# Performance work log

Hardware: AMD Instinct MI355X
Metric: run time of the kernel (lower is better)

The kernel has to match this reference:

```python
import jax, jax.numpy as jnp
import numpy as np

H = 768          # hidden_size
NH = 12          # num heads
HD = H // NH     # head dim
NEG = -1e9       # stand-in for -inf masked_fill (numerically safe)


def setup_inputs() -> dict:
    key = jax.random.key(0)
    ks = jax.random.split(key, 8)
    B, T = 4, 2048
    s = 0.02
    return {
        "hidden_states": jax.random.normal(ks[0], (B, T, H), jnp.float32),
        "attention_mask": jnp.zeros((B, 1, 1, T), jnp.float32),
        "Wq": jax.random.normal(ks[1], (H, H), jnp.float32) * s,
        "bq": jnp.zeros((H,), jnp.float32),
        "Wk": jax.random.normal(ks[2], (H, H), jnp.float32) * s,
        "bk": jnp.zeros((H,), jnp.float32),
        "Wv": jax.random.normal(ks[3], (H, H), jnp.float32) * s,
        "bv": jnp.zeros((H,), jnp.float32),
    }


def _split_heads(x):
    b, t, _ = x.shape
    return x.reshape(b, t, NH, HD).transpose(0, 2, 1, 3)  # b h t d


def reference(hidden_states, attention_mask, Wq, bq, Wk, bk, Wv, bv):
    q = _split_heads(hidden_states @ Wq.T + bq)
    k = _split_heads(hidden_states @ Wk.T + bk)
    v = _split_heads(hidden_states @ Wv.T + bv)
    T = q.shape[2]
    scores = jnp.einsum('bhid,bhjd->bhij', q, k) / jnp.sqrt(jnp.float32(HD))
    causal = jnp.tril(jnp.ones((T, T), bool))
    scores = jnp.where(causal, scores, NEG) + attention_mask
    probs = jax.nn.softmax(scores, axis=-1)
    out = jnp.einsum('bhij,bhjd->bhid', probs, v)
    b = out.shape[0]
    return out.transpose(0, 2, 1, 3).reshape(b, T, H)  # b t (h d)
```

## Files before the change

kernel.cpp:

```cpp
#include <hip/hip_runtime.h>
#include <hip/hip_bf16.h>

#define Tsz 2048
#define Hsz 768
#define NHsz 12
#define HDsz 64

typedef unsigned short u16;
typedef unsigned int u32;
typedef __attribute__((ext_vector_type(8))) short bf16x8;
typedef __attribute__((ext_vector_type(4))) float f32x4;
typedef __attribute__((ext_vector_type(4))) u16 u16x4;

__device__ __forceinline__ u16 f2bf(float f) {
    union { __hip_bfloat16 h; u16 u; } c;
    c.h = __float2bfloat16(f);
    return c.u;
}

__device__ __forceinline__ void glds16(const void* src, void* ldsbase) {
    __builtin_amdgcn_global_load_lds(
        (const __attribute__((address_space(1))) u32*)src,
        (__attribute__((address_space(3))) u32*)ldsbase, 16, 0, 0);
}

#define BAR() do { asm volatile("" ::: "memory"); \
                   __builtin_amdgcn_s_barrier();  \
                   asm volatile("" ::: "memory"); } while (0)

#define LDSFRAG(base, row, c) \
    (*(const bf16x8*)((const char*)(base) + (row)*128 + ((((c) << 4)) ^ (((row) & 7) << 4))))

__global__ __launch_bounds__(256) void to_bf16(
    const float* __restrict__ X,
    const float* __restrict__ Wq, const float* __restrict__ Wk,
    const float* __restrict__ Wv,
    u16* __restrict__ xb, u16* __restrict__ wb)
{
    const int bx = blockIdx.x, tid = threadIdx.x;
    const float* src;
    u16* dst;
    size_t off;
    if (bx < 768) {
        src = X; dst = xb;
        off = ((size_t)bx * 256 + tid) * 32;
    } else {
        int r = bx - 768;
        int wsel = r / 72, lr = r % 72;
        src = (wsel == 0) ? Wq : (wsel == 1) ? Wk : Wv;
        dst = wb + (size_t)wsel * (Hsz * Hsz);
        off = ((size_t)lr * 256 + tid) * 32;
    }
    #pragma unroll
    for (int c = 0; c < 4; ++c) {
        float4 a = *(const float4*)(src + off + c * 8);
        float4 b = *(const float4*)(src + off + c * 8 + 4);
        bf16x8 v;
        v[0] = (short)f2bf(a.x); v[1] = (short)f2bf(a.y);
        v[2] = (short)f2bf(a.z); v[3] = (short)f2bf(a.w);
        v[4] = (short)f2bf(b.x); v[5] = (short)f2bf(b.y);
        v[6] = (short)f2bf(b.z); v[7] = (short)f2bf(b.w);
        *(bf16x8*)(dst + off + c * 8) = v;
    }
}

__global__ __launch_bounds__(256) void qkv_gemm(
    const u16* __restrict__ xb, const u16* __restrict__ wb,
    const float* __restrict__ bq, const float* __restrict__ bk,
    const float* __restrict__ bv,
    u16* __restrict__ q_ws, u16* __restrict__ k_ws, u16* __restrict__ vt_ws)
{
    const int tid = threadIdx.x;
    const int w = tid >> 6, l = tid & 63, lg = l >> 4, lh = l & 15;
    const int nb = blockIdx.x;
    const int m0 = blockIdx.y * 128;
    const int z = nb / 6;
    const int n0l = (nb % 6) * 128;
    const u16* Wb = wb + (size_t)z * (Hsz * Hsz);
    const float* bias = (z == 0) ? bq : (z == 1) ? bk : bv;

    __shared__ __align__(16) u16 Xs[2][128 * 64];
    __shared__ __align__(16) u16 Ws[2][128 * 64];

    const int wm = w >> 1, wn = w & 1;

    f32x4 acc[4][4];
    #pragma unroll
    for (int i = 0; i < 4; ++i)
        #pragma unroll
        for (int j = 0; j < 4; ++j)
            acc[i][j] = (f32x4){0.f, 0.f, 0.f, 0.f};

    auto stage = [&](int buf, int k0) {
        #pragma unroll
        for (int p = 0; p < 4; ++p) {
            int id = w * 256 + p * 64 + l;
            int r = id >> 3, c8 = id & 7;
            int cswz = c8 ^ (r & 7);
            glds16(xb + (size_t)(m0 + r) * Hsz + k0 + cswz * 8,
                   &Xs[buf][(w * 256 + p * 64) * 8]);
            glds16(Wb + (size_t)(n0l + r) * Hsz + k0 + cswz * 8,
                   &Ws[buf][(w * 256 + p * 64) * 8]);
        }
    };

    stage(0, 0);
    asm volatile("s_waitcnt vmcnt(0)" ::: "memory");
    BAR();

    #pragma unroll 1
    for (int ks = 0; ks < 12; ++ks) {
        const int cur = ks & 1;
        if (ks < 11) {
            stage(cur ^ 1, (ks + 1) * 64);
            asm volatile("s_waitcnt vmcnt(8)" ::: "memory");
        } else {
            asm volatile("s_waitcnt vmcnt(0)" ::: "memory");
        }
        BAR();

        __builtin_amdgcn_s_setprio(1);
        #pragma unroll
        for (int s = 0; s < 2; ++s) {
            bf16x8 af[4], bfr[4];
            #pragma unroll
            for (int tq = 0; tq < 4; ++tq) {
                af[tq]  = LDSFRAG(Xs[cur], wm * 64 + tq * 16 + lh, 4 * s + lg);
                bfr[tq] = LDSFRAG(Ws[cur], wn * 64 + tq * 16 + lh, 4 * s + lg);
            }
            if (z <= 1) {
                #pragma unroll
                for (int mt = 0; mt < 4; ++mt)
                    #pragma unroll
                    for (int nt = 0; nt < 4; ++nt)
                        acc[mt][nt] = __builtin_amdgcn_mfma_f32_16x16x32_bf16(
                            bfr[nt], af[mt], acc[mt][nt], 0, 0, 0);
            } else {
                #pragma unroll
                for (int mt = 0; mt < 4; ++mt)
                    #pragma unroll
                    for (int nt = 0; nt < 4; ++nt)
                        acc[mt][nt] = __builtin_amdgcn_mfma_f32_16x16x32_bf16(
                            af[mt], bfr[nt], acc[mt][nt], 0, 0, 0);
            }
        }
        __builtin_amdgcn_s_setprio(0);
        BAR();
    }

    if (z <= 1) {
        u16* outp = (z == 0) ? q_ws : k_ws;
        #pragma unroll
        for (int mt = 0; mt < 4; ++mt) {
            int m = m0 + wm * 64 + mt * 16 + lh;
            int bb = m >> 11, t = m & 2047;
            #pragma unroll
            for (int nt = 0; nt < 4; ++nt) {
                int nbase = n0l + wn * 64 + nt * 16 + lg * 4;
                int hh = nbase >> 6, d0 = nbase & 63;
                f32x4 b4 = *(const f32x4*)(bias + nbase);
                u16x4 pk;
                #pragma unroll
                for (int r = 0; r < 4; ++r) pk[r] = f2bf(acc[mt][nt][r] + b4[r]);
                *(u16x4*)(outp + ((size_t)(bb * NHsz + hh) * Tsz + t) * HDsz + d0) = pk;
            }
        }
    } else {
        #pragma unroll
        for (int nt = 0; nt < 4; ++nt) {
            int nloc = n0l + wn * 64 + nt * 16 + lh;
            float bval = bias[nloc];
            int hh = nloc >> 6, d = nloc & 63;
            #pragma unroll
            for (int mt = 0; mt < 4; ++mt) {
                int t0m = m0 + wm * 64 + mt * 16 + lg * 4;
                int bb = t0m >> 11, t0 = t0m & 2047;
                u16x4 pk;
                #pragma unroll
                for (int r = 0; r < 4; ++r) pk[r] = f2bf(acc[mt][nt][r] + bval);
                *(u16x4*)(vt_ws + ((size_t)(bb * NHsz + hh) * HDsz + d) * Tsz + t0) = pk;
            }
        }
    }
}

__global__ __launch_bounds__(256) void attn_mfma(
    const u16* __restrict__ q_ws, const u16* __restrict__ k_ws,
    const u16* __restrict__ vt_ws, const float* __restrict__ am,
    float* __restrict__ out)
{
    const int tid = threadIdx.x;
    const int w = tid >> 6, l = tid & 63, lg = l >> 4, lh = l & 15;
    const int wg = blockIdx.x;
    const int swz = (wg & 7) * 96 + (wg >> 3);
    const int bx = swz & 15;
    const int grp = swz >> 4;
    const int h = grp % NHsz, b = grp / NHsz;
    const int bh = b * NHsz + h;

    const u16* Qb = q_ws + (size_t)bh * Tsz * HDsz;
    const u16* Kb = k_ws + (size_t)bh * Tsz * HDsz;
    const u16* Vb = vt_ws + (size_t)bh * HDsz * Tsz;
    const float* amb = am + (size_t)b * Tsz;

    __shared__ __align__(16) u16 Ks[2][64 * 64];
    __shared__ __align__(16) u16 Vs[2][64 * 64];
    __shared__ __align__(16) u16 Ps[4][16 * 64];
    __shared__ __align__(16) float ambs[Tsz];

    const float LOG2E  = 1.44269504f;
    const float SCALE2 = 0.125f * 1.44269504f;
    const f32x4 zero4 = {0.f, 0.f, 0.f, 0.f};
    u16* myP = &Ps[w][0];
    const int srcbase = l & 0x30;
    const int qo = lg * 4;

    #pragma unroll
    for (int i = 0; i < 2; ++i)
        glds16(amb + (size_t)(i * 256 + tid) * 4, ambs + (i * 256 + w * 64) * 4);
    asm volatile("s_waitcnt vmcnt(0)" ::: "memory");
    __syncthreads();
    #pragma unroll
    for (int i = 0; i < 8; ++i) ambs[tid * 8 + i] *= LOG2E;
    __syncthreads();

    #pragma unroll 1
    for (int ph = 0; ph < 2; ++ph) {
        const int qt = (ph == 0) ? (16 + bx) : (15 - bx);
        const int q0 = qt * 64 + w * 16;
        const int qrow = q0 + lh;

        #pragma unroll
        for (int p = 0; p < 2; ++p) {
            int id = w * 128 + p * 64 + l;
            int r = id >> 3, c8 = id & 7;
            int cswz = c8 ^ (r & 7);
            glds16(Kb + (size_t)r * HDsz + cswz * 8, &Ks[0][(w * 128 + p * 64) * 8]);
            glds16(Vb + (size_t)r * Tsz + cswz * 8, &Vs[0][(w * 128 + p * 64) * 8]);
        }
        bf16x8 qf0 = *(const bf16x8*)(Qb + (size_t)(q0 + lh) * HDsz + lg * 8);
        bf16x8 qf1 = *(const bf16x8*)(Qb + (size_t)(q0 + lh) * HDsz + lg * 8 + 32);
        asm volatile("s_waitcnt vmcnt(0)" ::: "memory");
        BAR();

        f32x4 o[4];
        #pragma unroll
        for (int n = 0; n < 4; ++n) o[n] = zero4;
        float m2 = -1e30f, l2 = 0.f;

        #pragma unroll 1
        for (int kt = 0; kt <= qt; ++kt) {
            const int cur = kt & 1;
            const int kv0 = kt * 64;

            if (kt < qt) {
                const int kv1 = kv0 + 64;
                #pragma unroll
                for (int p = 0; p < 2; ++p) {
                    int id = w * 128 + p * 64 + l;
                    int r = id >> 3, c8 = id & 7;
                    int cswz = c8 ^ (r & 7);
                    glds16(Kb + (size_t)(kv1 + r) * HDsz + cswz * 8,
                           &Ks[cur ^ 1][(w * 128 + p * 64) * 8]);
                    glds16(Vb + (size_t)r * Tsz + kv1 + cswz * 8,
                           &Vs[cur ^ 1][(w * 128 + p * 64) * 8]);
                }
                asm volatile("s_waitcnt vmcnt(4)" ::: "memory");
            } else {
                asm volatile("s_waitcnt vmcnt(0)" ::: "memory");
            }
            BAR();

            const u16* Ksb = &Ks[cur][0];
            const u16* Vsb = &Vs[cur][0];
            const bool diag = (kt == qt);

            f32x4 st[4];
            __builtin_amdgcn_s_setprio(1);
            if (!diag) {
                #pragma unroll
                for (int n = 0; n < 4; ++n) {
                    int row = n * 16 + lh;
                    bf16x8 kf0 = LDSFRAG(Ksb, row, lg);
                    bf16x8 kf1 = LDSFRAG(Ksb, row, 4 + lg);
                    f32x4 c = __builtin_amdgcn_mfma_f32_16x16x32_bf16(kf0, qf0, zero4, 0, 0, 0);
                    st[n] = __builtin_amdgcn_mfma_f32_16x16x32_bf16(kf1, qf1, c, 0, 0, 0);
                }
            } else {
                #pragma unroll
                for (int n = 0; n < 4; ++n) {
                    st[n] = zero4;
                    if (n <= w) {
                        int row = n * 16 + lh;
                        bf16x8 kf0 = LDSFRAG(Ksb, row, lg);
                        bf16x8 kf1 = LDSFRAG(Ksb, row, 4 + lg);
                        f32x4 c = __builtin_amdgcn_mfma_f32_16x16x32_bf16(kf0, qf0, zero4, 0, 0, 0);
                        st[n] = __builtin_amdgcn_mfma_f32_16x16x32_bf16(kf1, qf1, c, 0, 0, 0);
                    }
                }
            }
            __builtin_amdgcn_s_setprio(0);

            float pvv[16];
            float mx = -1e30f;
            if (!diag) {
                #pragma unroll
                for (int n = 0; n < 4; ++n) {
                    f32x4 a4 = *(const f32x4*)(ambs + kv0 + n * 16 + lg * 4);
                    #pragma unroll
                    for (int r = 0; r < 4; ++r) {
                        float sv = fmaf(st[n][r], SCALE2, a4[r]);
                        pvv[n * 4 + r] = sv;
                        mx = fmaxf(mx, sv);
                    }
                }
            } else {
                #pragma unroll
                for (int n = 0; n < 4; ++n) {
                    f32x4 a4 = *(const f32x4*)(ambs + kv0 + n * 16 + lg * 4);
                    #pragma unroll
                    for (int r = 0; r < 4; ++r) {
                        int kvj = kv0 + n * 16 + lg * 4 + r;
                        float sv = (kvj > qrow) ? -1e30f : fmaf(st[n][r], SCALE2, a4[r]);
                        pvv[n * 4 + r] = sv;
                        mx = fmaxf(mx, sv);
                    }
                }
            }
            mx = fmaxf(mx, __shfl_xor(mx, 16));
            mx = fmaxf(mx, __shfl_xor(mx, 32));

            const bool norescale = __all(mx <= m2 + 8.0f);
            float mn = m2;
            if (!norescale) mn = fmaxf(m2, mx);

            float ps = 0.f;
            #pragma unroll
            for (int i = 0; i < 16; ++i) {
                float p = exp2f(pvv[i] - mn);
                pvv[i] = p;
                ps += p;
            }
            ps += __shfl_xor(ps, 16);
            ps += __shfl_xor(ps, 32);

            if (norescale) {
                l2 += ps;
            } else {
                float corr = exp2f(m2 - mn);
                m2 = mn;
                l2 = l2 * corr + ps;
                float co[4];
                #pragma unroll
                for (int r = 0; r < 4; ++r)
                    co[r] = __shfl(corr, srcbase | (qo + r));
                #pragma unroll
                for (int n = 0; n < 4; ++n)
                    #pragma unroll
                    for (int r = 0; r < 4; ++r)
                        o[n][r] *= co[r];
            }

            #pragma unroll
            for (int n = 0; n < 4; ++n) {
                u16x4 v;
                v[0] = f2bf(pvv[n * 4 + 0]); v[1] = f2bf(pvv[n * 4 + 1]);
                v[2] = f2bf(pvv[n * 4 + 2]); v[3] = f2bf(pvv[n * 4 + 3]);
                int chunk = 2 * n + (lg >> 1);
                int byteoff = lh * 128 + ((chunk ^ (lh & 7)) << 4) + ((lg & 1) << 3);
                *(u16x4*)((char*)myP + byteoff) = v;
            }

            const int smaxv = (diag && w < 2) ? 0 : 1;
            __builtin_amdgcn_s_setprio(1);
            #pragma unroll
            for (int s = 0; s < 2; ++s) {
                if (s <= smaxv) {
                    int chunk = (4 * s + lg) ^ (lh & 7);
                    bf16x8 pf = *(const bf16x8*)((const char*)myP + lh * 128 + (chunk << 4));
                    #pragma unroll
                    for (int n = 0; n < 4; ++n) {
                        bf16x8 vf = LDSFRAG(Vsb, n * 16 + lh, 4 * s + lg);
                        o[n] = __builtin_amdgcn_mfma_f32_16x16x32_bf16(pf, vf, o[n], 0, 0, 0);
                    }
                }
            }
            __builtin_amdgcn_s_setprio(0);
            BAR();
        }

        float linv[4];
        #pragma unroll
        for (int r = 0; r < 4; ++r)
            linv[r] = 1.0f / __shfl(l2, srcbase | (qo + r));
        float* ob = out + ((size_t)(b * Tsz + q0 + qo)) * Hsz + h * HDsz + lh;
        #pragma unroll
        for (int r = 0; r < 4; ++r)
            #pragma unroll
            for (int n = 0; n < 4; ++n)
                ob[r * Hsz + n * 16] = o[n][r] * linv[r];
    }
}

extern "C" void kernel_launch(void* const* d_in, const int* in_sizes, int n_in,
                              void* d_out, int out_size, void* d_ws, size_t ws_size,
                              hipStream_t stream) {
    const float* X  = (const float*)d_in[0];
    const float* am = (const float*)d_in[1];
    const float* Wq = (const float*)d_in[2];
    const float* bq = (const float*)d_in[3];
    const float* Wk = (const float*)d_in[4];
    const float* bk = (const float*)d_in[5];
    const float* Wv = (const float*)d_in[6];
    const float* bv = (const float*)d_in[7];
    float* out = (float*)d_out;

    const size_t per = (size_t)8192 * Hsz;
    u16* q_ws  = (u16*)d_ws;
    u16* k_ws  = q_ws + per;
    u16* vt_ws = k_ws + per;

    u16* xb = (u16*)d_out;
    u16* wb = xb + per;

    to_bf16<<<dim3(984), 256, 0, stream>>>(X, Wq, Wk, Wv, xb, wb);

    dim3 g1(18, 64);
    qkv_gemm<<<g1, 256, 0, stream>>>(xb, wb, bq, bk, bv, q_ws, k_ws, vt_ws);

    attn_mfma<<<dim3(768), 256, 0, stream>>>(q_ws, k_ws, vt_ws, am, out);
}
```

Before: 141.5 us.

## Split attention into one q-tile per block with 32-wide KV tiles

Each workgroup now handles a single 64-row query tile, replacing the paired long/short tiles used for causal load balancing, and the grid doubles to 1536 blocks ordered longest-first. The KV tile shrinks from 64 to 32 keys, with matching smaller LDS buffers and a 4-way swizzle for the V tile. Smaller tiles and a finer diagonal skip let warps avoid fully masked work and cut LDS use, which should allow more blocks per CU. The cost is twice as many barrier and softmax-rescale iterations per key range, and per-block tail imbalance now relies on the hardware scheduler.

New measurement: 181.3 us. +28.1%, slower.

```diff
diff --git a/kernel.cpp b/kernel.cpp
--- a/kernel.cpp
+++ b/kernel.cpp
@@ -30,6 +30,8 @@
 
 #define LDSFRAG(base, row, c) \
     (*(const bf16x8*)((const char*)(base) + (row)*128 + ((((c) << 4)) ^ (((row) & 7) << 4))))
+#define LDSFRAG32(base, row, c) \
+    (*(const bf16x8*)((const char*)(base) + (row)*64 + ((((c) ^ ((row) & 3)) << 4))))
 
 __global__ __launch_bounds__(256) void to_bf16(
     const float* __restrict__ X,
@@ -192,9 +194,9 @@
     const int tid = threadIdx.x;
     const int w = tid >> 6, l = tid & 63, lg = l >> 4, lh = l & 15;
     const int wg = blockIdx.x;
-    const int swz = (wg & 7) * 96 + (wg >> 3);
-    const int bx = swz & 15;
-    const int grp = swz >> 4;
+    const int swz = (wg & 7) * 192 + (wg >> 3);
+    const int grp = swz >> 5;
+    const int qt  = 31 - (swz & 31);
     const int h = grp % NHsz, b = grp / NHsz;
     const int bh = b * NHsz + h;
 
@@ -203,109 +205,89 @@
     const u16* Vb = vt_ws + (size_t)bh * HDsz * Tsz;
     const float* amb = am + (size_t)b * Tsz;
 
-    __shared__ __align__(16) u16 Ks[2][64 * 64];
-    __shared__ __align__(16) u16 Vs[2][64 * 64];
-    __shared__ __align__(16) u16 Ps[4][16 * 64];
+    __shared__ __align__(16) u16 Ks[2][32 * 64];
+    __shared__ __align__(16) u16 Vs[2][64 * 32];
+    __shared__ __align__(16) u16 Ps[4][16 * 32];
     __shared__ __align__(16) float ambs[Tsz];
 
+    const float SCALE2 = 0.125f * 1.44269504f;
     const float LOG2E  = 1.44269504f;
-    const float SCALE2 = 0.125f * 1.44269504f;
     const f32x4 zero4 = {0.f, 0.f, 0.f, 0.f};
     u16* myP = &Ps[w][0];
     const int srcbase = l & 0x30;
     const int qo = lg * 4;
 
+    const int q0 = qt * 64 + w * 16;
+    const int qrow = q0 + lh;
+    const int q0wmax = q0 + 15;
+    const int ktmax = 2 * qt + 1;
+
     #pragma unroll
     for (int i = 0; i < 2; ++i)
         glds16(amb + (size_t)(i * 256 + tid) * 4, ambs + (i * 256 + w * 64) * 4);
+    {
+        int id = w * 64 + l;
+        int r = id >> 3, c8 = id & 7;
+        glds16(Kb + (size_t)r * HDsz + (c8 ^ (r & 7)) * 8, &Ks[0][id * 8]);
+        int rv = id >> 2, c4 = id & 3;
+        glds16(Vb + (size_t)rv * Tsz + (c4 ^ (rv & 3)) * 8, &Vs[0][id * 8]);
+    }
+    bf16x8 qf0 = *(const bf16x8*)(Qb + (size_t)(q0 + lh) * HDsz + lg * 8);
+    bf16x8 qf1 = *(const bf16x8*)(Qb + (size_t)(q0 + lh) * HDsz + lg * 8 + 32);
     asm volatile("s_waitcnt vmcnt(0)" ::: "memory");
     __syncthreads();
     #pragma unroll
     for (int i = 0; i < 8; ++i) ambs[tid * 8 + i] *= LOG2E;
     __syncthreads();
 
+    f32x4 o[4];
+    #pragma unroll
+    for (int n = 0; n < 4; ++n) o[n] = zero4;
+    float m2 = -1e30f, l2 = 0.f;
+
     #pragma unroll 1
-    for (int ph = 0; ph < 2; ++ph) {
-        const int qt = (ph == 0) ? (16 + bx) : (15 - bx);
-        const int q0 = qt * 64 + w * 16;
-        const int qrow = q0 + lh;
-
-        #pragma unroll
-        for (int p = 0; p < 2; ++p) {
-            int id = w * 128 + p * 64 + l;
+    for (int kt = 0; kt <= ktmax; ++kt) {
+        const int cur = kt & 1;
+        const int kv0 = kt * 32;
+
+        if (kt < ktmax) {
+            const int kv1 = kv0 + 32;
+            int id = w * 64 + l;
             int r = id >> 3, c8 = id & 7;
-            int cswz = c8 ^ (r & 7);
-            glds16(Kb + (size_t)r * HDsz + cswz * 8, &Ks[0][(w * 128 + p * 64) * 8]);
-            glds16(Vb + (size_t)r * Tsz + cswz * 8, &Vs[0][(w * 128 + p * 64) * 8]);
-        }
-        bf16x8 qf0 = *(const bf16x8*)(Qb + (size_t)(q0 + lh) * HDsz + lg * 8);
-        bf16x8 qf1 = *(const bf16x8*)(Qb + (size_t)(q0 + lh) * HDsz + lg * 8 + 32);
-        asm volatile("s_waitcnt vmcnt(0)" ::: "memory");
+            glds16(Kb + (size_t)(kv1 + r) * HDsz + (c8 ^ (r & 7)) * 8,
+                   &Ks[cur ^ 1][id * 8]);
+            int rv = id >> 2, c4 = id & 3;
+            glds16(Vb + (size_t)rv * Tsz + kv1 + (c4 ^ (rv & 3)) * 8,
+                   &Vs[cur ^ 1][id * 8]);
+            asm volatile("s_waitcnt vmcnt(2)" ::: "memory");
+        } else {
+            asm volatile("s_waitcnt vmcnt(0)" ::: "memory");
+        }
         BAR();
 
-        f32x4 o[4];
-        #pragma unroll
-        for (int n = 0; n < 4; ++n) o[n] = zero4;
-        float m2 = -1e30f, l2 = 0.f;
-
-        #pragma unroll 1
-        for (int kt = 0; kt <= qt; ++kt) {
-            const int cur = kt & 1;
-            const int kv0 = kt * 64;
-
-            if (kt < qt) {
-                const int kv1 = kv0 + 64;
-                #pragma unroll
-                for (int p = 0; p < 2; ++p) {
-                    int id = w * 128 + p * 64 + l;
-                    int r = id >> 3, c8 = id & 7;
-                    int cswz = c8 ^ (r & 7);
-                    glds16(Kb + (size_t)(kv1 + r) * HDsz + cswz * 8,
-                           &Ks[cur ^ 1][(w * 128 + p * 64) * 8]);
-                    glds16(Vb + (size_t)r * Tsz + kv1 + cswz * 8,
-                           &Vs[cur ^ 1][(w * 128 + p * 64) * 8]);
-                }
-                asm volatile("s_waitcnt vmcnt(4)" ::: "memory");
-            } else {
-                asm volatile("s_waitcnt vmcnt(0)" ::: "memory");
-            }
-            BAR();
-
+        const bool haswork = (kv0 <= q0wmax);
+        if (haswork) {
             const u16* Ksb = &Ks[cur][0];
             const u16* Vsb = &Vs[cur][0];
-            const bool diag = (kt == qt);
-
-            f32x4 st[4];
+            const bool edge = (kt >= 2 * qt);
+
+            f32x4 st[2];
             __builtin_amdgcn_s_setprio(1);
-            if (!diag) {
-                #pragma unroll
-                for (int n = 0; n < 4; ++n) {
-                    int row = n * 16 + lh;
-                    bf16x8 kf0 = LDSFRAG(Ksb, row, lg);
-                    bf16x8 kf1 = LDSFRAG(Ksb, row, 4 + lg);
-                    f32x4 c = __builtin_amdgcn_mfma_f32_16x16x32_bf16(kf0, qf0, zero4, 0, 0, 0);
-                    st[n] = __builtin_amdgcn_mfma_f32_16x16x32_bf16(kf1, qf1, c, 0, 0, 0);
-                }
-            } else {
-                #pragma unroll
-                for (int n = 0; n < 4; ++n) {
-                    st[n] = zero4;
-                    if (n <= w) {
-                        int row = n * 16 + lh;
-                        bf16x8 kf0 = LDSFRAG(Ksb, row, lg);
-                        bf16x8 kf1 = LDSFRAG(Ksb, row, 4 + lg);
-                        f32x4 c = __builtin_amdgcn_mfma_f32_16x16x32_bf16(kf0, qf0, zero4, 0, 0, 0);
-                        st[n] = __builtin_amdgcn_mfma_f32_16x16x32_bf16(kf1, qf1, c, 0, 0, 0);
-                    }
-                }
+            #pragma unroll
+            for (int n = 0; n < 2; ++n) {
+                int row = n * 16 + lh;
+                bf16x8 kf0 = LDSFRAG(Ksb, row, lg);
+                bf16x8 kf1 = LDSFRAG(Ksb, row, 4 + lg);
+                f32x4 c = __builtin_amdgcn_mfma_f32_16x16x32_bf16(kf0, qf0, zero4, 0, 0, 0);
+                st[n] = __builtin_amdgcn_mfma_f32_16x16x32_bf16(kf1, qf1, c, 0, 0, 0);
             }
             __builtin_amdgcn_s_setprio(0);
 
-            float pvv[16];
+            float pvv[8];
             float mx = -1e30f;
-            if (!diag) {
-                #pragma unroll
-                for (int n = 0; n < 4; ++n) {
+            if (!edge) {
+                #pragma unroll
+                for (int n = 0; n < 2; ++n) {
                     f32x4 a4 = *(const f32x4*)(ambs + kv0 + n * 16 + lg * 4);
                     #pragma unroll
                     for (int r = 0; r < 4; ++r) {
@@ -316,7 +298,7 @@
                 }
             } else {
                 #pragma unroll
-                for (int n = 0; n < 4; ++n) {
+                for (int n = 0; n < 2; ++n) {
                     f32x4 a4 = *(const f32x4*)(ambs + kv0 + n * 16 + lg * 4);
                     #pragma unroll
                     for (int r = 0; r < 4; ++r) {
@@ -336,7 +318,7 @@
 
             float ps = 0.f;
             #pragma unroll
-            for (int i = 0; i < 16; ++i) {
+            for (int i = 0; i < 8; ++i) {
                 float p = exp2f(pvv[i] - mn);
                 pvv[i] = p;
                 ps += p;
@@ -362,44 +344,40 @@
             }
 
             #pragma unroll
-            for (int n = 0; n < 4; ++n) {
+            for (int n = 0; n < 2; ++n) {
                 u16x4 v;
                 v[0] = f2bf(pvv[n * 4 + 0]); v[1] = f2bf(pvv[n * 4 + 1]);
                 v[2] = f2bf(pvv[n * 4 + 2]); v[3] = f2bf(pvv[n * 4 + 3]);
                 int chunk = 2 * n + (lg >> 1);
-                int byteoff = lh * 128 + ((chunk ^ (lh & 7)) << 4) + ((lg & 1) << 3);
+                int byteoff = lh * 64 + ((chunk ^ (lh & 3)) << 4) + ((lg & 1) << 3);
                 *(u16x4*)((char*)myP + byteoff) = v;
             }
 
-            const int smaxv = (diag && w < 2) ? 0 : 1;
             __builtin_amdgcn_s_setprio(1);
-            #pragma unroll
-            for (int s = 0; s < 2; ++s) {
-                if (s <= smaxv) {
-                    int chunk = (4 * s + lg) ^ (lh & 7);
-                    bf16x8 pf = *(const bf16x8*)((const char*)myP + lh * 128 + (chunk << 4));
-                    #pragma unroll
-                    for (int n = 0; n < 4; ++n) {
-                        bf16x8 vf = LDSFRAG(Vsb, n * 16 + lh, 4 * s + lg);
-                        o[n] = __builtin_amdgcn_mfma_f32_16x16x32_bf16(pf, vf, o[n], 0, 0, 0);
-                    }
+            {
+                int chunk = lg ^ (lh & 3);
+                bf16x8 pf = *(const bf16x8*)((const char*)myP + lh * 64 + (chunk << 4));
+                #pragma unroll
+                for (int n = 0; n < 4; ++n) {
+                    bf16x8 vf = LDSFRAG32(Vsb, n * 16 + lh, lg);
+                    o[n] = __builtin_amdgcn_mfma_f32_16x16x32_bf16(pf, vf, o[n], 0, 0, 0);
                 }
             }
             __builtin_amdgcn_s_setprio(0);
-            BAR();
-        }
-
-        float linv[4];
-        #pragma unroll
-        for (int r = 0; r < 4; ++r)
-            linv[r] = 1.0f / __shfl(l2, srcbase | (qo + r));
-        float* ob = out + ((size_t)(b * Tsz + q0 + qo)) * Hsz + h * HDsz + lh;
-        #pragma unroll
-        for (int r = 0; r < 4; ++r)
-            #pragma unroll
-            for (int n = 0; n < 4; ++n)
-                ob[r * Hsz + n * 16] = o[n][r] * linv[r];
-    }
+        }
+        BAR();
+    }
+
+    float linv[4];
+    #pragma unroll
+    for (int r = 0; r < 4; ++r)
+        linv[r] = 1.0f / __shfl(l2, srcbase | (qo + r));
+    float* ob = out + ((size_t)(b * Tsz + q0 + qo)) * Hsz + h * HDsz + lh;
+    #pragma unroll
+    for (int r = 0; r < 4; ++r)
+        #pragma unroll
+        for (int n = 0; n < 4; ++n)
+            ob[r * Hsz + n * 16] = o[n][r] * linv[r];
 }
 
 extern "C" void kernel_launch(void* const* d_in, const int* in_sizes, int n_in,
@@ -428,5 +406,5 @@
     dim3 g1(18, 64);
     qkv_gemm<<<g1, 256, 0, stream>>>(xb, wb, bq, bk, bv, q_ws, k_ws, vt_ws);
 
-    attn_mfma<<<dim3(768), 256, 0, stream>>>(q_ws, k_ws, vt_ws, am, out);
-}
+    attn_mfma<<<dim3(1536), 256, 0, stream>>>(q_ws, k_ws, vt_ws, am, out);
+}
```

## Merge both causal query-tile phases into one KV sweep sharing K/V tiles

Applied to the files above, without the earlier changes.

The two sequential phases, one for the high query tile and one for the low query tile, are replaced by a single loop over KV tiles. Each loaded K/V tile is used by both query tiles while the low tile is still in range. This roughly halves global-to-LDS K/V traffic and barrier count for the low tile, and drops the second prologue. In exchange each wave holds two sets of accumulators, running max/sum and Q fragments, which raises register pressure and may reduce occupancy.

After: 141.7 us. About the same (+0.1%).

```diff
diff --git a/kernel.cpp b/kernel.cpp
--- a/kernel.cpp
+++ b/kernel.cpp
@@ -215,190 +215,209 @@
     const int srcbase = l & 0x30;
     const int qo = lg * 4;
 
+    const int qt_hi = 16 + bx, qt_lo = 15 - bx;
+    const int q0h = qt_hi * 64 + w * 16;
+    const int q0l = qt_lo * 64 + w * 16;
+    const int qrow_h = q0h + lh, qrow_l = q0l + lh;
+
     #pragma unroll
     for (int i = 0; i < 2; ++i)
         glds16(amb + (size_t)(i * 256 + tid) * 4, ambs + (i * 256 + w * 64) * 4);
+    #pragma unroll
+    for (int p = 0; p < 2; ++p) {
+        int id = w * 128 + p * 64 + l;
+        int r = id >> 3, c8 = id & 7;
+        int cswz = c8 ^ (r & 7);
+        glds16(Kb + (size_t)r * HDsz + cswz * 8, &Ks[0][(w * 128 + p * 64) * 8]);
+        glds16(Vb + (size_t)r * Tsz + cswz * 8, &Vs[0][(w * 128 + p * 64) * 8]);
+    }
+    bf16x8 qfh0 = *(const bf16x8*)(Qb + (size_t)(q0h + lh) * HDsz + lg * 8);
+    bf16x8 qfh1 = *(const bf16x8*)(Qb + (size_t)(q0h + lh) * HDsz + lg * 8 + 32);
+    bf16x8 qfl0 = *(const bf16x8*)(Qb + (size_t)(q0l + lh) * HDsz + lg * 8);
+    bf16x8 qfl1 = *(const bf16x8*)(Qb + (size_t)(q0l + lh) * HDsz + lg * 8 + 32);
     asm volatile("s_waitcnt vmcnt(0)" ::: "memory");
     __syncthreads();
     #pragma unroll
     for (int i = 0; i < 8; ++i) ambs[tid * 8 + i] *= LOG2E;
     __syncthreads();
 
-    #pragma unroll 1
-    for (int ph = 0; ph < 2; ++ph) {
-        const int qt = (ph == 0) ? (16 + bx) : (15 - bx);
-        const int q0 = qt * 64 + w * 16;
-        const int qrow = q0 + lh;
-
-        #pragma unroll
-        for (int p = 0; p < 2; ++p) {
-            int id = w * 128 + p * 64 + l;
-            int r = id >> 3, c8 = id & 7;
-            int cswz = c8 ^ (r & 7);
-            glds16(Kb + (size_t)r * HDsz + cswz * 8, &Ks[0][(w * 128 + p * 64) * 8]);
-            glds16(Vb + (size_t)r * Tsz + cswz * 8, &Vs[0][(w * 128 + p * 64) * 8]);
-        }
-        bf16x8 qf0 = *(const bf16x8*)(Qb + (size_t)(q0 + lh) * HDsz + lg * 8);
-        bf16x8 qf1 = *(const bf16x8*)(Qb + (size_t)(q0 + lh) * HDsz + lg * 8 + 32);
-        asm volatile("s_waitcnt vmcnt(0)" ::: "memory");
-        BAR();
-
-        f32x4 o[4];
-        #pragma unroll
-        for (int n = 0; n < 4; ++n) o[n] = zero4;
-        float m2 = -1e30f, l2 = 0.f;
-
-        #pragma unroll 1
-        for (int kt = 0; kt <= qt; ++kt) {
-            const int cur = kt & 1;
-            const int kv0 = kt * 64;
-
-            if (kt < qt) {
-                const int kv1 = kv0 + 64;
-                #pragma unroll
-                for (int p = 0; p < 2; ++p) {
-                    int id = w * 128 + p * 64 + l;
-                    int r = id >> 3, c8 = id & 7;
-                    int cswz = c8 ^ (r & 7);
-                    glds16(Kb + (size_t)(kv1 + r) * HDsz + cswz * 8,
-                           &Ks[cur ^ 1][(w * 128 + p * 64) * 8]);
-                    glds16(Vb + (size_t)r * Tsz + kv1 + cswz * 8,
-                           &Vs[cur ^ 1][(w * 128 + p * 64) * 8]);
-                }
-                asm volatile("s_waitcnt vmcnt(4)" ::: "memory");
-            } else {
-                asm volatile("s_waitcnt vmcnt(0)" ::: "memory");
-            }
-            BAR();
-
-            const u16* Ksb = &Ks[cur][0];
-            const u16* Vsb = &Vs[cur][0];
-            const bool diag = (kt == qt);
-
-            f32x4 st[4];
-            __builtin_amdgcn_s_setprio(1);
-            if (!diag) {
-                #pragma unroll
-                for (int n = 0; n < 4; ++n) {
+    f32x4 oh[4], ol[4];
+    #pragma unroll
+    for (int n = 0; n < 4; ++n) { oh[n] = zero4; ol[n] = zero4; }
+    float m2h = -1e30f, l2h = 0.f, m2l = -1e30f, l2l = 0.f;
+
+    auto phase = [&](const bf16x8& qf0, const bf16x8& qf1, int qrow,
+                     f32x4* o, float& m2, float& l2,
+                     bool diag, const u16* Ksb, const u16* Vsb, int kv0) {
+        f32x4 st[4];
+        __builtin_amdgcn_s_setprio(1);
+        if (!diag) {
+            #pragma unroll
+            for (int n = 0; n < 4; ++n) {
+                int row = n * 16 + lh;
+                bf16x8 kf0 = LDSFRAG(Ksb, row, lg);
+                bf16x8 kf1 = LDSFRAG(Ksb, row, 4 + lg);
+                f32x4 c = __builtin_amdgcn_mfma_f32_16x16x32_bf16(kf0, qf0, zero4, 0, 0, 0);
+                st[n] = __builtin_amdgcn_mfma_f32_16x16x32_bf16(kf1, qf1, c, 0, 0, 0);
+            }
+        } else {
+            #pragma unroll
+            for (int n = 0; n < 4; ++n) {
+                st[n] = zero4;
+                if (n <= w) {
                     int row = n * 16 + lh;
                     bf16x8 kf0 = LDSFRAG(Ksb, row, lg);
                     bf16x8 kf1 = LDSFRAG(Ksb, row, 4 + lg);
                     f32x4 c = __builtin_amdgcn_mfma_f32_16x16x32_bf16(kf0, qf0, zero4, 0, 0, 0);
                     st[n] = __builtin_amdgcn_mfma_f32_16x16x32_bf16(kf1, qf1, c, 0, 0, 0);
                 }
-            } else {
+            }
+        }
+        __builtin_amdgcn_s_setprio(0);
+
+        float pvv[16];
+        float mx = -1e30f;
+        if (!diag) {
+            #pragma unroll
+            for (int n = 0; n < 4; ++n) {
+                f32x4 a4 = *(const f32x4*)(ambs + kv0 + n * 16 + lg * 4);
+                #pragma unroll
+                for (int r = 0; r < 4; ++r) {
+                    float sv = fmaf(st[n][r], SCALE2, a4[r]);
+                    pvv[n * 4 + r] = sv;
+                    mx = fmaxf(mx, sv);
+                }
+            }
+        } else {
+            #pragma unroll
+            for (int n = 0; n < 4; ++n) {
+                f32x4 a4 = *(const f32x4*)(ambs + kv0 + n * 16 + lg * 4);
+                #pragma unroll
+                for (int r = 0; r < 4; ++r) {
+                    int kvj = kv0 + n * 16 + lg * 4 + r;
+                    float sv = (kvj > qrow) ? -1e30f : fmaf(st[n][r], SCALE2, a4[r]);
+                    pvv[n * 4 + r] = sv;
+                    mx = fmaxf(mx, sv);
+                }
+            }
+        }
+        mx = fmaxf(mx, __shfl_xor(mx, 16));
+        mx = fmaxf(mx, __shfl_xor(mx, 32));
+
+        const bool norescale = __all(mx <= m2 + 8.0f);
+        float mn = m2;
+        if (!norescale) mn = fmaxf(m2, mx);
+
+        float ps = 0.f;
+        #pragma unroll
+        for (int i = 0; i < 16; ++i) {
+            float p = exp2f(pvv[i] - mn);
+            pvv[i] = p;
+            ps += p;
+        }
+        ps += __shfl_xor(ps, 16);
+        ps += __shfl_xor(ps, 32);
+
+        if (norescale) {
+            l2 += ps;
+        } else {
+            float corr = exp2f(m2 - mn);
+            m2 = mn;
+            l2 = l2 * corr + ps;
+            float co[4];
+            #pragma unroll
+            for (int r = 0; r < 4; ++r)
+                co[r] = __shfl(corr, srcbase | (qo + r));
+            #pragma unroll
+            for (int n = 0; n < 4; ++n)
+                #pragma unroll
+                for (int r = 0; r < 4; ++r)
+                    o[n][r] *= co[r];
+        }
+
+        #pragma unroll
+        for (int n = 0; n < 4; ++n) {
+            u16x4 v;
+            v[0] = f2bf(pvv[n * 4 + 0]); v[1] = f2bf(pvv[n * 4 + 1]);
+            v[2] = f2bf(pvv[n * 4 + 2]); v[3] = f2bf(pvv[n * 4 + 3]);
+            int chunk = 2 * n + (lg >> 1);
+            int byteoff = lh * 128 + ((chunk ^ (lh & 7)) << 4) + ((lg & 1) << 3);
+            *(u16x4*)((char*)myP + byteoff) = v;
+        }
+
+        const int smaxv = (diag && w < 2) ? 0 : 1;
+        __builtin_amdgcn_s_setprio(1);
+        #pragma unroll
+        for (int s = 0; s < 2; ++s) {
+            if (s <= smaxv) {
+                int chunk = (4 * s + lg) ^ (lh & 7);
+                bf16x8 pf = *(const bf16x8*)((const char*)myP + lh * 128 + (chunk << 4));
                 #pragma unroll
                 for (int n = 0; n < 4; ++n) {
-                    st[n] = zero4;
-                    if (n <= w) {
-                        int row = n * 16 + lh;
-                        bf16x8 kf0 = LDSFRAG(Ksb, row, lg);
-                        bf16x8 kf1 = LDSFRAG(Ksb, row, 4 + lg);
-                        f32x4 c = __builtin_amdgcn_mfma_f32_16x16x32_bf16(kf0, qf0, zero4, 0, 0, 0);
-                        st[n] = __builtin_amdgcn_mfma_f32_16x16x32_bf16(kf1, qf1, c, 0, 0, 0);
-                    }
+                    bf16x8 vf = LDSFRAG(Vsb, n * 16 + lh, 4 * s + lg);
+                    o[n] = __builtin_amdgcn_mfma_f32_16x16x32_bf16(pf, vf, o[n], 0, 0, 0);
                 }
             }
-            __builtin_amdgcn_s_setprio(0);
-
-            float pvv[16];
-            float mx = -1e30f;
-            if (!diag) {
-                #pragma unroll
-                for (int n = 0; n < 4; ++n) {
-                    f32x4 a4 = *(const f32x4*)(ambs + kv0 + n * 16 + lg * 4);
-                    #pragma unroll
-                    for (int r = 0; r < 4; ++r) {
-                        float sv = fmaf(st[n][r], SCALE2, a4[r]);
-                        pvv[n * 4 + r] = sv;
-                        mx = fmaxf(mx, sv);
-                    }
-                }
-            } else {
-                #pragma unroll
-                for (int n = 0; n < 4; ++n) {
-                    f32x4 a4 = *(const f32x4*)(ambs + kv0 + n * 16 + lg * 4);
-                    #pragma unroll
-                    for (int r = 0; r < 4; ++r) {
-                        int kvj = kv0 + n * 16 + lg * 4 + r;
-                        float sv = (kvj > qrow) ? -1e30f : fmaf(st[n][r], SCALE2, a4[r]);
-                        pvv[n * 4 + r] = sv;
-                        mx = fmaxf(mx, sv);
-                    }
-                }
-            }
-            mx = fmaxf(mx, __shfl_xor(mx, 16));
-            mx = fmaxf(mx, __shfl_xor(mx, 32));
-
-            const bool norescale = __all(mx <= m2 + 8.0f);
-            float mn = m2;
-            if (!norescale) mn = fmaxf(m2, mx);
-
-            float ps = 0.f;
-            #pragma unroll
-            for (int i = 0; i < 16; ++i) {
-                float p = exp2f(pvv[i] - mn);
-                pvv[i] = p;
-                ps += p;
-            }
-            ps += __shfl_xor(ps, 16);
-            ps += __shfl_xor(ps, 32);
-
-            if (norescale) {
-                l2 += ps;
-            } else {
-                float corr = exp2f(m2 - mn);
-                m2 = mn;
-                l2 = l2 * corr + ps;
-                float co[4];
-                #pragma unroll
-                for (int r = 0; r < 4; ++r)
-                    co[r] = __shfl(corr, srcbase | (qo + r));
-                #pragma unroll
-                for (int n = 0; n < 4; ++n)
-                    #pragma unroll
-                    for (int r = 0; r < 4; ++r)
-                        o[n][r] *= co[r];
-            }
-
-            #pragma unroll
-            for (int n = 0; n < 4; ++n) {
-                u16x4 v;
-                v[0] = f2bf(pvv[n * 4 + 0]); v[1] = f2bf(pvv[n * 4 + 1]);
-                v[2] = f2bf(pvv[n * 4 + 2]); v[3] = f2bf(pvv[n * 4 + 3]);
-                int chunk = 2 * n + (lg >> 1);
-                int byteoff = lh * 128 + ((chunk ^ (lh & 7)) << 4) + ((lg & 1) << 3);
-                *(u16x4*)((char*)myP + byteoff) = v;
-            }
-
-            const int smaxv = (diag && w < 2) ? 0 : 1;
-            __builtin_amdgcn_s_setprio(1);
-            #pragma unroll
-            for (int s = 0; s < 2; ++s) {
-                if (s <= smaxv) {
-                    int chunk = (4 * s + lg) ^ (lh & 7);
-                    bf16x8 pf = *(const bf16x8*)((const char*)myP + lh * 128 + (chunk << 4));
-                    #pragma unroll
-                    for (int n = 0; n < 4; ++n) {
-                        bf16x8 vf = LDSFRAG(Vsb, n * 16 + lh, 4 * s + lg);
-                        o[n] = __builtin_amdgcn_mfma_f32_16x16x32_bf16(pf, vf, o[n], 0, 0, 0);
-                    }
-                }
-            }
-            __builtin_amdgcn_s_setprio(0);
-            BAR();
-        }
-
+        }
+        __builtin_amdgcn_s_setprio(0);
+    };
+
+    #pragma unroll 1
+    for (int kt = 0; kt <= qt_hi; ++kt) {
+        const int cur = kt & 1;
+        const int kv0 = kt * 64;
+
+        if (kt < qt_hi) {
+            const int kv1 = kv0 + 64;
+            #pragma unroll
+            for (int p = 0; p < 2; ++p) {
+                int id = w * 128 + p * 64 + l;
+                int r = id >> 3, c8 = id & 7;
+                int cswz = c8 ^ (r & 7);
+                glds16(Kb + (size_t)(kv1 + r) * HDsz + cswz * 8,
+                       &Ks[cur ^ 1][(w * 128 + p * 64) * 8]);
+                glds16(Vb + (size_t)r * Tsz + kv1 + cswz * 8,
+                       &Vs[cur ^ 1][(w * 128 + p * 64) * 8]);
+            }
+            asm volatile("s_waitcnt vmcnt(4)" ::: "memory");
+        } else {
+            asm volatile("s_waitcnt vmcnt(0)" ::: "memory");
+        }
+        BAR();
+
+        const u16* Ksb = &Ks[cur][0];
+        const u16* Vsb = &Vs[cur][0];
+
+        phase(qfh0, qfh1, qrow_h, oh, m2h, l2h, kt == qt_hi, Ksb, Vsb, kv0);
+        if (kt <= qt_lo)
+            phase(qfl0, qfl1, qrow_l, ol, m2l, l2l, kt == qt_lo, Ksb, Vsb, kv0);
+
+        BAR();
+    }
+
+    {
         float linv[4];
         #pragma unroll
         for (int r = 0; r < 4; ++r)
-            linv[r] = 1.0f / __shfl(l2, srcbase | (qo + r));
-        float* ob = out + ((size_t)(b * Tsz + q0 + qo)) * Hsz + h * HDsz + lh;
+            linv[r] = 1.0f / __shfl(l2h, srcbase | (qo + r));
+        float* ob = out + ((size_t)(b * Tsz + q0h + qo)) * Hsz + h * HDsz + lh;
         #pragma unroll
         for (int r = 0; r < 4; ++r)
             #pragma unroll
             for (int n = 0; n < 4; ++n)
-                ob[r * Hsz + n * 16] = o[n][r] * linv[r];
+                ob[r * Hsz + n * 16] = oh[n][r] * linv[r];
+    }
+    {
+        float linv[4];
+        #pragma unroll
+        for (int r = 0; r < 4; ++r)
+            linv[r] = 1.0f / __shfl(l2l, srcbase | (qo + r));
+        float* ob = out + ((size_t)(b * Tsz + q0l + qo)) * Hsz + h * HDsz + lh;
+        #pragma unroll
+        for (int r = 0; r < 4; ++r)
+            #pragma unroll
+            for (int n = 0; n < 4; ++n)
+                ob[r * Hsz + n * 16] = ol[n][r] * linv[r];
     }
 }
 
```
